# Kernel tuning notes

Hardware: AMD Instinct MI355X
Metric: run time of the kernel (lower is better)

Reference implementation:

```python
import jax, jax.numpy as jnp
import numpy as np

N, E = 50000, 640000
DIN, DH, DOUT = 128, 256, 128


def _glorot(k, i, o):
    return jax.random.normal(k, (i, o), jnp.float32) / np.sqrt(i)


def setup_inputs() -> dict:
    key = jax.random.key(0)
    ks = jax.random.split(key, 12)
    return {
        "x": jax.random.normal(ks[0], (N, DIN), jnp.float32),
        "edge_index": jax.random.randint(ks[1], (2, E), 0, N, dtype=jnp.int32),
        # SAGEConv 1: in -> hidden (lin_l on aggregated w/ bias, lin_r on root)
        "W1l": _glorot(ks[2], DIN, DH), "b1l": jnp.zeros((DH,), jnp.float32), "W1r": _glorot(ks[3], DIN, DH),
        "g1": jnp.ones((DH,), jnp.float32), "be1": jnp.zeros((DH,), jnp.float32),
        # skip projection (in != hidden)
        "Wsk": _glorot(ks[4], DIN, DH), "bsk": jnp.zeros((DH,), jnp.float32),
        # SAGEConv 2: hidden -> hidden
        "W2l": _glorot(ks[5], DH, DH), "b2l": jnp.zeros((DH,), jnp.float32), "W2r": _glorot(ks[6], DH, DH),
        "g2": jnp.ones((DH,), jnp.float32), "be2": jnp.zeros((DH,), jnp.float32),
        # SAGEConv 3: hidden -> out
        "W3l": _glorot(ks[7], DH, DOUT), "b3l": jnp.zeros((DOUT,), jnp.float32), "W3r": _glorot(ks[8], DH, DOUT),
    }


def _sage_conv(x, src, dst, Wl, bl, Wr, n):
    # mean aggregation of source features into destination nodes
    msg = x[src]                                                 # [E, d]
    agg = jax.ops.segment_sum(msg, dst, num_segments=n)          # [N, d]
    cnt = jax.ops.segment_sum(jnp.ones((src.shape[0],), x.dtype), dst, num_segments=n)
    agg = agg / jnp.maximum(cnt, 1.0)[:, None]
    return agg @ Wl + bl + x @ Wr


def _layernorm(x, g, b):
    mu = jnp.mean(x, axis=-1, keepdims=True)
    var = jnp.mean((x - mu) ** 2, axis=-1, keepdims=True)
    return (x - mu) * jax.lax.rsqrt(var + 1e-5) * g + b


def reference(x, edge_index, W1l, b1l, W1r, g1, be1, Wsk, bsk,
              W2l, b2l, W2r, g2, be2, W3l, b3l, W3r):
    src, dst = edge_index[0], edge_index[1]
    n = x.shape[0]
    # layer 0: conv -> LN -> relu -> (dropout p=0, eval) -> skip via projection
    h = _sage_conv(x, src, dst, W1l, b1l, W1r, n)
    h = jax.nn.relu(_layernorm(h, g1, be1))
    h = h + (x @ Wsk + bsk)
    # layer 1: conv -> LN -> relu -> residual add (shapes match)
    h2 = _sage_conv(h, src, dst, W2l, b2l, W2r, n)
    h2 = jax.nn.relu(_layernorm(h2, g2, be2)) + h
    # final conv (no norm/act)
    return _sage_conv(h2, src, dst, W3l, b3l, W3r, n)
```

## Files before the change

### kernel.cpp

```cpp
#include <hip/hip_runtime.h>


typedef float floatx4 __attribute__((ext_vector_type(4)));
typedef float floatx2 __attribute__((ext_vector_type(2)));
typedef short bf16x8 __attribute__((ext_vector_type(8)));

__device__ inline unsigned short f2bf(float f) {
    unsigned u = __float_as_uint(f);
    unsigned r = (u + 0x7fffu + ((u >> 16) & 1u)) >> 16;
    return (unsigned short)r;
}
__device__ inline float bf2f_lo(unsigned v) { return __uint_as_float(v << 16); }
__device__ inline float bf2f_hi(unsigned v) { return __uint_as_float(v & 0xffff0000u); }

__device__ inline void gl_lds16(const void* g, void* l) {
    __builtin_amdgcn_global_load_lds((const __attribute__((address_space(1))) unsigned int*)g,
                                     (__attribute__((address_space(3))) unsigned int*)l,
                                     16, 0, 0);
}

__global__ void hist_kernel(const int* __restrict__ dst, int* __restrict__ cnt, int E) {
    int i = blockIdx.x * blockDim.x + threadIdx.x;
    if (i < E) atomicAdd(&cnt[dst[i]], 1);
}

#define SCAN_CHUNK 2048

__global__ __launch_bounds__(256) void scan_blocksums(const int* __restrict__ cnt,
                                                      int* __restrict__ bsum, int N) {
    __shared__ int sh[256];
    int t = threadIdx.x;
    int base = blockIdx.x * SCAN_CHUNK + t * 8;
    int s = 0;
#pragma unroll
    for (int i = 0; i < 8; i++) {
        int idx = base + i;
        if (idx < N) s += cnt[idx];
    }
    sh[t] = s;
    __syncthreads();
    for (int off = 1; off < 256; off <<= 1) {
        int v = (t >= off) ? sh[t - off] : 0;
        __syncthreads();
        sh[t] += v;
        __syncthreads();
    }
    if (t == 255) bsum[blockIdx.x] = sh[255];
}

__global__ __launch_bounds__(256) void scan_bsums(const int* __restrict__ bsum,
                                                  int* __restrict__ boff, int NB,
                                                  int* __restrict__ rowptr, int N, int E) {
    __shared__ int sh[256];
    int t = threadIdx.x;
    int v = (t < NB) ? bsum[t] : 0;
    sh[t] = v;
    __syncthreads();
    for (int off = 1; off < 256; off <<= 1) {
        int u = (t >= off) ? sh[t - off] : 0;
        __syncthreads();
        sh[t] += u;
        __syncthreads();
    }
    if (t < NB) boff[t] = sh[t] - v;
    if (t == 0) rowptr[N] = E;
}

__global__ __launch_bounds__(256) void scan_final(const int* __restrict__ cnt,
                                                  const int* __restrict__ boff,
                                                  int* __restrict__ rowptr,
                                                  int* __restrict__ cursor,
                                                  float* __restrict__ invdeg, int N) {
    __shared__ int sh[256];
    int t = threadIdx.x;
    int base = blockIdx.x * SCAN_CHUNK + t * 8;
    int c[8];
    int s = 0;
#pragma unroll
    for (int i = 0; i < 8; i++) {
        int idx = base + i;
        c[i] = (idx < N) ? cnt[idx] : 0;
        s += c[i];
    }
    sh[t] = s;
    __syncthreads();
    for (int off = 1; off < 256; off <<= 1) {
        int v = (t >= off) ? sh[t - off] : 0;
        __syncthreads();
        sh[t] += v;
        __syncthreads();
    }
    int run = boff[blockIdx.x] + sh[t] - s;
#pragma unroll
    for (int i = 0; i < 8; i++) {
        int idx = base + i;
        if (idx < N) {
            rowptr[idx] = run;
            cursor[idx] = run;
            invdeg[idx] = 1.0f / (float)(c[i] > 1 ? c[i] : 1);
            run += c[i];
        }
    }
}

__global__ void scatter_kernel(const int* __restrict__ src, const int* __restrict__ dst,
                               int* __restrict__ cursor, int* __restrict__ col, int E) {
    int i = blockIdx.x * blockDim.x + threadIdx.x;
    if (i < E) {
        int p = atomicAdd(&cursor[dst[i]], 1);
        col[p] = src[i];
    }
}

__global__ void prep_weights(const float* __restrict__ W1l, const float* __restrict__ W1r,
                             const float* __restrict__ Wsk, const float* __restrict__ W2l,
                             const float* __restrict__ W2r, const float* __restrict__ W3l,
                             const float* __restrict__ W3r, const float* __restrict__ b1l,
                             const float* __restrict__ bsk,
                             unsigned short* __restrict__ WtC, unsigned short* __restrict__ Wt2,
                             unsigned short* __restrict__ Wt3, float* __restrict__ biasC) {
    int i = blockIdx.x * blockDim.x + threadIdx.x;
    if (i < 32768) {
        int k = i >> 8, n = i & 255;
        WtC[n * 256 + k] = f2bf(W1l[i]);
    } else if (i < 65536) {
        int j = i - 32768, k = j >> 8, n = j & 255;
        WtC[n * 256 + 128 + k] = f2bf(W1r[j]);
    } else if (i < 98304) {
        int j = i - 65536, k = j >> 8, n = j & 255;
        WtC[(256 + n) * 256 + 128 + k] = f2bf(Wsk[j]);
    } else if (i < 131072) {
        int j = i - 98304, k = j >> 8, n = j & 255;
        WtC[(256 + n) * 256 + k] = 0;
    } else if (i < 196608) {
        int j = i - 131072, k = j >> 8, n = j & 255;
        Wt2[n * 512 + k] = f2bf(W2l[j]);
    } else if (i < 262144) {
        int j = i - 196608, k = j >> 8, n = j & 255;
        Wt2[n * 512 + 256 + k] = f2bf(W2r[j]);
    } else if (i < 294912) {
        int j = i - 262144, k = j >> 7, n = j & 127;
        Wt3[n * 256 + k] = f2bf(W3l[j]);
    } else if (i < 327680) {
        int j = i - 294912, k = j >> 7, n = j & 127;
        Wt3[(128 + n) * 256 + k] = f2bf(W3r[j]);
    } else if (i < 328192) {
        int j = i - 327680;
        biasC[j] = (j < 256) ? b1l[j] : bsk[j - 256];
    }
}

__global__ void cvt_x2(const float* __restrict__ x, unsigned short* __restrict__ A1cat,
                       unsigned char* __restrict__ X8, int total32) {
    int i = blockIdx.x * blockDim.x + threadIdx.x;
    if (i >= total32) return;
    int r = i >> 5, c4 = (i & 31) * 4;
    float4 v = *(const float4*)(x + (size_t)r * 128 + c4);
    ushort4 o;
    o.x = f2bf(v.x); o.y = f2bf(v.y); o.z = f2bf(v.z); o.w = f2bf(v.w);
    *(ushort4*)(A1cat + (size_t)r * 256 + 128 + c4) = o;
    unsigned wpk = 0;
    wpk = __builtin_amdgcn_cvt_pk_fp8_f32(v.x, v.y, wpk, false);
    wpk = __builtin_amdgcn_cvt_pk_fp8_f32(v.z, v.w, wpk, true);
    *(unsigned*)(X8 + (size_t)r * 128 + c4) = wpk;
}

__device__ inline void accum_fp8(uint2 v, float m, float* a) {
    floatx2 p;
    p = __builtin_amdgcn_cvt_pk_f32_fp8(v.x, false); a[0] = fmaf(m, p.x, a[0]); a[1] = fmaf(m, p.y, a[1]);
    p = __builtin_amdgcn_cvt_pk_f32_fp8(v.x, true);  a[2] = fmaf(m, p.x, a[2]); a[3] = fmaf(m, p.y, a[3]);
    p = __builtin_amdgcn_cvt_pk_f32_fp8(v.y, false); a[4] = fmaf(m, p.x, a[4]); a[5] = fmaf(m, p.y, a[5]);
    p = __builtin_amdgcn_cvt_pk_f32_fp8(v.y, true);  a[6] = fmaf(m, p.x, a[6]); a[7] = fmaf(m, p.y, a[7]);
}

__global__ __launch_bounds__(256) void agg_fp8_128(const int* __restrict__ rowptr,
                                                   const int* __restrict__ col,
                                                   const float* __restrict__ invdeg,
                                                   const unsigned char* __restrict__ X8,
                                                   unsigned short* __restrict__ out, int ostride, int N) {
    int wid = (blockIdx.x * blockDim.x + threadIdx.x) >> 6;
    int lane = threadIdx.x & 63;
    if (wid >= N) return;
    int q = lane >> 4;
    int sub = lane & 15;
    const unsigned char* Xo = X8 + sub * 8;
    int s = rowptr[wid], e = rowptr[wid + 1];
    float a[8] = {0.f, 0.f, 0.f, 0.f, 0.f, 0.f, 0.f, 0.f};
    for (int j = s + q; j < e; j += 16) {
        int j1 = (j + 4 < e) ? j + 4 : j;
        int j2 = (j + 8 < e) ? j + 8 : j;
        int j3 = (j + 12 < e) ? j + 12 : j;
        float m1 = (j + 4 < e) ? 1.f : 0.f;
        float m2 = (j + 8 < e) ? 1.f : 0.f;
        float m3 = (j + 12 < e) ? 1.f : 0.f;
        int c0 = col[j], c1 = col[j1], c2 = col[j2], c3 = col[j3];
        uint2 v0 = *(const uint2*)(Xo + (size_t)c0 * 128);
        uint2 v1 = *(const uint2*)(Xo + (size_t)c1 * 128);
        uint2 v2 = *(const uint2*)(Xo + (size_t)c2 * 128);
        uint2 v3 = *(const uint2*)(Xo + (size_t)c3 * 128);
        accum_fp8(v0, 1.f, a);
        accum_fp8(v1, m1, a);
        accum_fp8(v2, m2, a);
        accum_fp8(v3, m3, a);
    }
#pragma unroll
    for (int i = 0; i < 8; i++) {
        a[i] += __shfl_xor(a[i], 16, 64);
        a[i] += __shfl_xor(a[i], 32, 64);
    }
    if (q == 0) {
        float inv = invdeg[wid];
        uint4 o;
        o.x = (unsigned)f2bf(a[0] * inv) | ((unsigned)f2bf(a[1] * inv) << 16);
        o.y = (unsigned)f2bf(a[2] * inv) | ((unsigned)f2bf(a[3] * inv) << 16);
        o.z = (unsigned)f2bf(a[4] * inv) | ((unsigned)f2bf(a[5] * inv) << 16);
        o.w = (unsigned)f2bf(a[6] * inv) | ((unsigned)f2bf(a[7] * inv) << 16);
        *(uint4*)(out + (size_t)wid * ostride + sub * 8) = o;
    }
}

__global__ __launch_bounds__(256) void agg_fp8_256(const int* __restrict__ rowptr,
                                                   const int* __restrict__ col,
                                                   const float* __restrict__ invdeg,
                                                   const unsigned char* __restrict__ H8,
                                                   unsigned short* __restrict__ out, int ostride, int N) {
    int wid = (blockIdx.x * blockDim.x + threadIdx.x) >> 6;
    int lane = threadIdx.x & 63;
    if (wid >= N) return;
    int half = lane >> 5;
    int sub = lane & 31;
    const unsigned char* Ho = H8 + sub * 8;
    int s = rowptr[wid], e = rowptr[wid + 1];
    float a[8] = {0.f, 0.f, 0.f, 0.f, 0.f, 0.f, 0.f, 0.f};
    for (int j = s + half; j < e; j += 8) {
        int j1 = (j + 2 < e) ? j + 2 : j;
        int j2 = (j + 4 < e) ? j + 4 : j;
        int j3 = (j + 6 < e) ? j + 6 : j;
        float m1 = (j + 2 < e) ? 1.f : 0.f;
        float m2 = (j + 4 < e) ? 1.f : 0.f;
        float m3 = (j + 6 < e) ? 1.f : 0.f;
        int c0 = col[j], c1 = col[j1], c2 = col[j2], c3 = col[j3];
        uint2 v0 = *(const uint2*)(Ho + (size_t)c0 * 256);
        uint2 v1 = *(const uint2*)(Ho + (size_t)c1 * 256);
        uint2 v2 = *(const uint2*)(Ho + (size_t)c2 * 256);
        uint2 v3 = *(const uint2*)(Ho + (size_t)c3 * 256);
        accum_fp8(v0, 1.f, a);
        accum_fp8(v1, m1, a);
        accum_fp8(v2, m2, a);
        accum_fp8(v3, m3, a);
    }
#pragma unroll
    for (int i = 0; i < 8; i++) a[i] += __shfl_xor(a[i], 32, 64);
    if (half == 0) {
        float inv = invdeg[wid];
        uint4 o;
        o.x = (unsigned)f2bf(a[0] * inv) | ((unsigned)f2bf(a[1] * inv) << 16);
        o.y = (unsigned)f2bf(a[2] * inv) | ((unsigned)f2bf(a[3] * inv) << 16);
        o.z = (unsigned)f2bf(a[4] * inv) | ((unsigned)f2bf(a[5] * inv) << 16);
        o.w = (unsigned)f2bf(a[6] * inv) | ((unsigned)f2bf(a[7] * inv) << 16);
        *(uint4*)(out + (size_t)wid * ostride + sub * 8) = o;
    }
}

__global__ __launch_bounds__(256) void agg_final_v3(const int* __restrict__ rowptr,
                                                    const int* __restrict__ col,
                                                    const float* __restrict__ invdeg,
                                                    const unsigned short* __restrict__ T,
                                                    const float* __restrict__ R,
                                                    float* __restrict__ out, int N) {
    int wid = (blockIdx.x * blockDim.x + threadIdx.x) >> 6;
    int lane = threadIdx.x & 63;
    if (wid >= N) return;
    int half = lane >> 5;
    int sub = lane & 31;
    const unsigned short* To = T + sub * 4;
    int s = rowptr[wid], e = rowptr[wid + 1];
    float a0 = 0.f, a1 = 0.f, a2 = 0.f, a3 = 0.f;
    for (int j = s + half; j < e; j += 8) {
        int j1 = (j + 2 < e) ? j + 2 : j;
        int j2 = (j + 4 < e) ? j + 4 : j;
        int j3 = (j + 6 < e) ? j + 6 : j;
        float m1 = (j + 2 < e) ? 1.f : 0.f;
        float m2 = (j + 4 < e) ? 1.f : 0.f;
        float m3 = (j + 6 < e) ? 1.f : 0.f;
        int c0 = col[j], c1 = col[j1], c2 = col[j2], c3 = col[j3];
        uint2 v0 = *(const uint2*)(To + (size_t)c0 * 128);
        uint2 v1 = *(const uint2*)(To + (size_t)c1 * 128);
        uint2 v2 = *(const uint2*)(To + (size_t)c2 * 128);
        uint2 v3 = *(const uint2*)(To + (size_t)c3 * 128);
        a0 += bf2f_lo(v0.x); a1 += bf2f_hi(v0.x); a2 += bf2f_lo(v0.y); a3 += bf2f_hi(v0.y);
        a0 = fmaf(m1, bf2f_lo(v1.x), a0); a1 = fmaf(m1, bf2f_hi(v1.x), a1);
        a2 = fmaf(m1, bf2f_lo(v1.y), a2); a3 = fmaf(m1, bf2f_hi(v1.y), a3);
        a0 = fmaf(m2, bf2f_lo(v2.x), a0); a1 = fmaf(m2, bf2f_hi(v2.x), a1);
        a2 = fmaf(m2, bf2f_lo(v2.y), a2); a3 = fmaf(m2, bf2f_hi(v2.y), a3);
        a0 = fmaf(m3, bf2f_lo(v3.x), a0); a1 = fmaf(m3, bf2f_hi(v3.x), a1);
        a2 = fmaf(m3, bf2f_lo(v3.y), a2); a3 = fmaf(m3, bf2f_hi(v3.y), a3);
    }
    a0 += __shfl_xor(a0, 32, 64);
    a1 += __shfl_xor(a1, 32, 64);
    a2 += __shfl_xor(a2, 32, 64);
    a3 += __shfl_xor(a3, 32, 64);
    if (half == 0) {
        float inv = invdeg[wid];
        float4 r = *(const float4*)(R + (size_t)wid * 128 + sub * 4);
        float4 o;
        o.x = a0 * inv + r.x;
        o.y = a1 * inv + r.y;
        o.z = a2 * inv + r.z;
        o.w = a3 * inv + r.w;
        *(float4*)(out + (size_t)wid * 128 + sub * 4) = o;
    }
}

template <int KIT, int NP, int SPLIT>
__global__ __launch_bounds__(256) void gemm_lds2(const unsigned short* __restrict__ A, int lda,
                                                 const unsigned short* __restrict__ B, int ldb,
                                                 const float* __restrict__ bias,
                                                 unsigned short* __restrict__ C0, int ldc0,
                                                 float* __restrict__ C1, int M) {
    constexpr int STAGE = 128 * 64 * 2;
    constexpr int SMEM_SZ = (STAGE * (1 + NP) > 34816) ? STAGE * (1 + NP) : 34816;
    __shared__ __align__(16) char smem[SMEM_SZ];
    unsigned short* sA = (unsigned short*)smem;
    int t = threadIdx.x;
    int lane = t & 63, w = t >> 6;
    int bm = blockIdx.x * 128;
    int bn0 = blockIdx.y * 128 * NP;
    int wm = (w >> 1) * 64, wn = (w & 1) * 64;
    int m16 = lane & 15, kq = lane >> 4;

    floatx4 acc[NP][4][4];
#pragma unroll
    for (int p = 0; p < NP; p++)
#pragma unroll
        for (int i = 0; i < 4; i++)
#pragma unroll
            for (int j = 0; j < 4; j++) acc[p][i][j] = (floatx4){0.f, 0.f, 0.f, 0.f};

    const int c_row = t >> 3;
    const int kc = (t & 7) ^ (c_row & 7);
    const int srcOff = kc * 8;
    const int fsw = (m16 & 7);

    for (int kt = 0; kt < KIT; kt++) {
        int k0 = kt * 64;
#pragma unroll
        for (int i = 0; i < 4; i++) {
            int rowA = bm + i * 32 + c_row;
            if (rowA > M - 1) rowA = M - 1;
            gl_lds16(A + (size_t)rowA * lda + k0 + srcOff, (void*)&sA[(size_t)(i * 256 + t) * 8]);
#pragma unroll
            for (int p = 0; p < NP; p++)
                gl_lds16(B + (size_t)(bn0 + p * 128 + i * 32 + c_row) * ldb + k0 + srcOff,
                         (void*)&sA[(size_t)((p + 1) * 128 * 64) + (size_t)(i * 256 + t) * 8]);
        }
        __syncthreads();
#pragma unroll
        for (int ks = 0; ks < 2; ks++) {
            int kcl = (ks << 2) | kq;
            bf16x8 af[4];
#pragma unroll
            for (int mi = 0; mi < 4; mi++)
                af[mi] = *(const bf16x8*)&sA[(wm + mi * 16 + m16) * 64 + (kcl ^ fsw) * 8];
#pragma unroll
            for (int p = 0; p < NP; p++) {
                const unsigned short* sB = sA + (p + 1) * 128 * 64;
                bf16x8 bfr[4];
#pragma unroll
                for (int ni = 0; ni < 4; ni++)
                    bfr[ni] = *(const bf16x8*)&sB[(wn + ni * 16 + m16) * 64 + (kcl ^ fsw) * 8];
#pragma unroll
                for (int mi = 0; mi < 4; mi++)
#pragma unroll
                    for (int ni = 0; ni < 4; ni++)
                        acc[p][mi][ni] =
                            __builtin_amdgcn_mfma_f32_16x16x32_bf16(af[mi], bfr[ni], acc[p][mi][ni], 0, 0, 0);
            }
        }
        __syncthreads();
    }

    float* wb = (float*)smem + w * (64 * 34);
#pragma unroll
    for (int p = 0; p < NP; p++) {
        const bool isF32 = (SPLIT == 1 && p == 1);
        const float* bp = (SPLIT == 0) ? (bias + bn0 + p * 128) : ((p == 0) ? nullptr : bias);
#pragma unroll
        for (int h = 0; h < 2; h++) {
#pragma unroll
            for (int nj = 0; nj < 2; nj++) {
                int ni = h * 2 + nj;
#pragma unroll
                for (int mi = 0; mi < 4; mi++)
#pragma unroll
                    for (int r = 0; r < 4; r++)
                        wb[(mi * 16 + kq * 4 + r) * 34 + nj * 16 + m16] = acc[p][mi][ni][r];
            }
            asm volatile("s_waitcnt lgkmcnt(0)" ::: "memory");
            if (!isF32) {
                int rsub = lane >> 2, c8 = (lane & 3) * 8;
                int ldc = (SPLIT == 0) ? ldc0 : 128;
                int lcol = wn + h * 32 + c8;
                int colbase = ((SPLIT == 0) ? bn0 + p * 128 : 0) + lcol;
                float bv[8];
#pragma unroll
                for (int j = 0; j < 8; j++) bv[j] = bp ? bp[lcol + j] : 0.f;
#pragma unroll
                for (int it = 0; it < 4; it++) {
                    int rr = it * 16 + rsub;
                    int grow = bm + wm + rr;
                    float v0 = wb[rr * 34 + c8 + 0] + bv[0];
                    float v1 = wb[rr * 34 + c8 + 1] + bv[1];
                    float v2 = wb[rr * 34 + c8 + 2] + bv[2];
                    float v3 = wb[rr * 34 + c8 + 3] + bv[3];
                    float v4 = wb[rr * 34 + c8 + 4] + bv[4];
                    float v5 = wb[rr * 34 + c8 + 5] + bv[5];
                    float v6 = wb[rr * 34 + c8 + 6] + bv[6];
                    float v7 = wb[rr * 34 + c8 + 7] + bv[7];
                    uint4 o;
                    o.x = (unsigned)f2bf(v0) | ((unsigned)f2bf(v1) << 16);
                    o.y = (unsigned)f2bf(v2) | ((unsigned)f2bf(v3) << 16);
                    o.z = (unsigned)f2bf(v4) | ((unsigned)f2bf(v5) << 16);
                    o.w = (unsigned)f2bf(v6) | ((unsigned)f2bf(v7) << 16);
                    if (grow < M) *(uint4*)(C0 + (size_t)grow * ldc + colbase) = o;
                }
            } else {
                int rsub = lane >> 3, c4 = (lane & 7) * 4;
                int gcol = wn + h * 32 + c4;
                float bv[4];
#pragma unroll
                for (int j = 0; j < 4; j++) bv[j] = bp[gcol + j];
#pragma unroll
                for (int it = 0; it < 8; it++) {
                    int rr = it * 8 + rsub;
                    int grow = bm + wm + rr;
                    float4 o;
                    o.x = wb[rr * 34 + c4 + 0] + bv[0];
                    o.y = wb[rr * 34 + c4 + 1] + bv[1];
                    o.z = wb[rr * 34 + c4 + 2] + bv[2];
                    o.w = wb[rr * 34 + c4 + 3] + bv[3];
                    if (grow < M) *(float4*)(C1 + (size_t)grow * 128 + gcol) = o;
                }
            }
            asm volatile("s_waitcnt lgkmcnt(0)" ::: "memory");
        }
    }
}

__global__ __launch_bounds__(256) void ln_fuse2(const unsigned short* __restrict__ u, int ustride,
                                                const unsigned short* __restrict__ a, int astride,
                                                const float* __restrict__ g, const float* __restrict__ b,
                                                unsigned short* __restrict__ out, int ostride,
                                                unsigned char* __restrict__ h8, int N) {
    int row = (blockIdx.x * blockDim.x + threadIdx.x) >> 6;
    int lane = threadIdx.x & 63;
    if (row >= N) return;
    uint2 uv = *(const uint2*)(u + (size_t)row * ustride + lane * 4);
    float v0 = bf2f_lo(uv.x), v1 = bf2f_hi(uv.x), v2 = bf2f_lo(uv.y), v3 = bf2f_hi(uv.y);
    float s = (v0 + v1) + (v2 + v3);
    float sq = (v0 * v0 + v1 * v1) + (v2 * v2 + v3 * v3);
    for (int off = 1; off < 64; off <<= 1) {
        s += __shfl_xor(s, off, 64);
        sq += __shfl_xor(sq, off, 64);
    }
    float mu = s * (1.f / 256.f);
    float var = sq * (1.f / 256.f) - mu * mu;
    float rs = rsqrtf(var + 1e-5f);
    float4 gv = *(const float4*)(g + lane * 4);
    float4 bv = *(const float4*)(b + lane * 4);
    uint2 av = *(const uint2*)(a + (size_t)row * astride + lane * 4);
    float a0 = bf2f_lo(av.x), a1 = bf2f_hi(av.x), a2 = bf2f_lo(av.y), a3 = bf2f_hi(av.y);
    float o0 = fmaxf((v0 - mu) * rs * gv.x + bv.x, 0.f) + a0;
    float o1 = fmaxf((v1 - mu) * rs * gv.y + bv.y, 0.f) + a1;
    float o2 = fmaxf((v2 - mu) * rs * gv.z + bv.z, 0.f) + a2;
    float o3 = fmaxf((v3 - mu) * rs * gv.w + bv.w, 0.f) + a3;
    ushort4 o;
    o.x = f2bf(o0); o.y = f2bf(o1); o.z = f2bf(o2); o.w = f2bf(o3);
    *(ushort4*)(out + (size_t)row * ostride + lane * 4) = o;
    if (h8) {
        unsigned wpk = 0;
        wpk = __builtin_amdgcn_cvt_pk_fp8_f32(o0, o1, wpk, false);
        wpk = __builtin_amdgcn_cvt_pk_fp8_f32(o2, o3, wpk, true);
        *(unsigned*)(h8 + (size_t)row * 256 + lane * 4) = wpk;
    }
}

extern "C" void kernel_launch(void* const* d_in, const int* in_sizes, int n_in,
                              void* d_out, int out_size, void* d_ws, size_t ws_size,
                              hipStream_t stream) {
    const float* x   = (const float*)d_in[0];
    const int*   ei  = (const int*)d_in[1];
    const float* W1l = (const float*)d_in[2];
    const float* b1l = (const float*)d_in[3];
    const float* W1r = (const float*)d_in[4];
    const float* g1  = (const float*)d_in[5];
    const float* be1 = (const float*)d_in[6];
    const float* Wsk = (const float*)d_in[7];
    const float* bsk = (const float*)d_in[8];
    const float* W2l = (const float*)d_in[9];
    const float* b2l = (const float*)d_in[10];
    const float* W2r = (const float*)d_in[11];
    const float* g2  = (const float*)d_in[12];
    const float* be2 = (const float*)d_in[13];
    const float* W3l = (const float*)d_in[14];
    const float* b3l = (const float*)d_in[15];
    const float* W3r = (const float*)d_in[16];

    const int N = in_sizes[0] / 128;
    const int E = in_sizes[1] / 2;
    const int* src = ei;
    const int* dst = ei + E;

    char* p = (char*)d_ws;
    auto alloc = [&](size_t bytes) {
        void* r = (void*)p;
        p += (bytes + 255) & ~(size_t)255;
        return r;
    };
    int*   cnt    = (int*)alloc(sizeof(int) * N);
    int*   rowptr = (int*)alloc(sizeof(int) * (N + 1));
    int*   cursor = (int*)alloc(sizeof(int) * N);
    float* invdeg = (float*)alloc(sizeof(float) * N);
    int*   col    = (int*)alloc(sizeof(int) * E);
    int*   bsum   = (int*)alloc(sizeof(int) * 256);
    int*   boff   = (int*)alloc(sizeof(int) * 256);
    unsigned short* A1cat = (unsigned short*)alloc(sizeof(short) * (size_t)N * 256);
    unsigned short* A2cat = (unsigned short*)alloc(sizeof(short) * (size_t)N * 512);
    unsigned short* U1    = (unsigned short*)alloc(sizeof(short) * (size_t)N * 512);
    float* r3 = (float*)alloc(sizeof(float) * (size_t)N * 128);
    unsigned char* H8 = (unsigned char*)alloc((size_t)N * 256);
    unsigned char* X8 = (unsigned char*)alloc((size_t)N * 128);
    unsigned short* WtC = (unsigned short*)alloc(sizeof(short) * 512 * 256);
    unsigned short* Wt2 = (unsigned short*)alloc(sizeof(short) * 256 * 512);
    unsigned short* Wt3 = (unsigned short*)alloc(sizeof(short) * 256 * 256);
    float* biasC = (float*)alloc(sizeof(float) * 512);
    unsigned short* t3 = A1cat;
    unsigned short* u2 = U1;

    hipMemsetAsync(cnt, 0, sizeof(int) * N, stream);
    hist_kernel<<<(E + 255) / 256, 256, 0, stream>>>(dst, cnt, E);
    int NB = (N + SCAN_CHUNK - 1) / SCAN_CHUNK;
    scan_blocksums<<<NB, 256, 0, stream>>>(cnt, bsum, N);
    scan_bsums<<<1, 256, 0, stream>>>(bsum, boff, NB, rowptr, N, E);
    scan_final<<<NB, 256, 0, stream>>>(cnt, boff, rowptr, cursor, invdeg, N);
    scatter_kernel<<<(E + 255) / 256, 256, 0, stream>>>(src, dst, cursor, col, E);

    prep_weights<<<(328192 + 255) / 256, 256, 0, stream>>>(W1l, W1r, Wsk, W2l, W2r, W3l, W3r,
                                                           b1l, bsk, WtC, Wt2, Wt3, biasC);
    cvt_x2<<<((N * 32) + 255) / 256, 256, 0, stream>>>(x, A1cat, X8, N * 32);

    int aggBlocks = (N + 3) / 4;
    int mBlocks = (N + 127) / 128;

    agg_fp8_128<<<aggBlocks, 256, 0, stream>>>(rowptr, col, invdeg, X8, A1cat, 256, N);
    gemm_lds2<4, 2, 0><<<dim3(mBlocks, 2), 256, 0, stream>>>(A1cat, 256, WtC, 256, biasC, U1, 512, nullptr, N);
    ln_fuse2<<<aggBlocks, 256, 0, stream>>>(U1, 512, U1 + 256, 512, g1, be1, A2cat + 256, 512, H8, N);

    agg_fp8_256<<<aggBlocks, 256, 0, stream>>>(rowptr, col, invdeg, H8, A2cat, 512, N);
    gemm_lds2<8, 2, 0><<<dim3(mBlocks, 1), 256, 0, stream>>>(A2cat, 512, Wt2, 512, b2l, u2, 256, nullptr, N);
    ln_fuse2<<<aggBlocks, 256, 0, stream>>>(u2, 256, A2cat + 256, 512, g2, be2, A2cat, 512, nullptr, N);

    gemm_lds2<4, 2, 1><<<dim3(mBlocks, 1), 256, 0, stream>>>(A2cat, 512, Wt3, 256, b3l, t3, 128, r3, N);
    agg_final_v3<<<aggBlocks, 256, 0, stream>>>(rowptr, col, invdeg, t3, r3, (float*)d_out, N);
}
```

Measured before the change: 384.3 us.

## Fuse LayerNorm/ReLU/residual epilogue into GEMM with full-width 512-thread tiles

```diff
diff --git a/kernel.cpp b/kernel.cpp
--- a/kernel.cpp
+++ b/kernel.cpp
@@ -312,176 +312,176 @@
     }
 }
 
-template <int KIT, int NP, int SPLIT>
-__global__ __launch_bounds__(256) void gemm_lds2(const unsigned short* __restrict__ A, int lda,
-                                                 const unsigned short* __restrict__ B, int ldb,
-                                                 const float* __restrict__ bias,
-                                                 unsigned short* __restrict__ C0, int ldc0,
-                                                 float* __restrict__ C1, int M) {
-    constexpr int STAGE = 128 * 64 * 2;
-    constexpr int SMEM_SZ = (STAGE * (1 + NP) > 34816) ? STAGE * (1 + NP) : 34816;
-    __shared__ __align__(16) char smem[SMEM_SZ];
-    unsigned short* sA = (unsigned short*)smem;
+template <int KIT, int NPAN, int MODE>
+__global__ __launch_bounds__(512) void gemm_fused(
+    const unsigned short* __restrict__ A, int lda,
+    const unsigned short* __restrict__ B, int ldb,
+    const float* __restrict__ bias,
+    const float* __restrict__ gamma, const float* __restrict__ beta,
+    const unsigned short* __restrict__ resid,
+    unsigned short* __restrict__ outb,
+    unsigned char* __restrict__ h8,
+    float* __restrict__ outf, int M) {
+    constexpr int COLS = NPAN * 256;
+    constexpr int LNW = COLS + 8;
+    constexpr int STAGE_E = 128 * 64;
+    constexpr int STAGE_F = 2 * STAGE_E / 2;
+    constexpr int SMEM_F = (STAGE_F > 32 * LNW) ? STAGE_F : 32 * LNW;
+    __shared__ __align__(16) float smemf[SMEM_F];
+    unsigned short* sbase = (unsigned short*)smemf;
+
     int t = threadIdx.x;
     int lane = t & 63, w = t >> 6;
     int bm = blockIdx.x * 128;
-    int bn0 = blockIdx.y * 128 * NP;
-    int wm = (w >> 1) * 64, wn = (w & 1) * 64;
+    int wm = (w & 1) * 64, wn = (w >> 1) * 64;
     int m16 = lane & 15, kq = lane >> 4;
 
-    floatx4 acc[NP][4][4];
-#pragma unroll
-    for (int p = 0; p < NP; p++)
+    floatx4 acc[NPAN][4][4];
+#pragma unroll
+    for (int p = 0; p < NPAN; p++)
 #pragma unroll
         for (int i = 0; i < 4; i++)
 #pragma unroll
             for (int j = 0; j < 4; j++) acc[p][i][j] = (floatx4){0.f, 0.f, 0.f, 0.f};
 
-    const int c_row = t >> 3;
-    const int kc = (t & 7) ^ (c_row & 7);
-    const int srcOff = kc * 8;
-    const int fsw = (m16 & 7);
-
+    const int s_row0 = t >> 3;
+    const int s_j = t & 7;
+
+    auto stage = [&](int kt, int bsel) {
+        unsigned short* s = sbase + bsel * STAGE_E;
+        int k0 = kt * 64;
+#pragma unroll
+        for (int i = 0; i < 2; i++) {
+            int row = s_row0 + i * 64;
+            int kc = s_j ^ (row & 7);
+            int rowA = bm + row;
+            if (rowA > M - 1) rowA = M - 1;
+            gl_lds16(A + (size_t)rowA * lda + k0 + kc * 8, (void*)&s[(size_t)(i * 512 + t) * 8]);
+        }
+    };
+
+    stage(0, 0);
+    __syncthreads();
     for (int kt = 0; kt < KIT; kt++) {
-        int k0 = kt * 64;
-#pragma unroll
-        for (int i = 0; i < 4; i++) {
-            int rowA = bm + i * 32 + c_row;
-            if (rowA > M - 1) rowA = M - 1;
-            gl_lds16(A + (size_t)rowA * lda + k0 + srcOff, (void*)&sA[(size_t)(i * 256 + t) * 8]);
-#pragma unroll
-            for (int p = 0; p < NP; p++)
-                gl_lds16(B + (size_t)(bn0 + p * 128 + i * 32 + c_row) * ldb + k0 + srcOff,
-                         (void*)&sA[(size_t)((p + 1) * 128 * 64) + (size_t)(i * 256 + t) * 8]);
-        }
-        __syncthreads();
+        if (kt + 1 < KIT) stage(kt + 1, (kt & 1) ^ 1);
+        const unsigned short* sA = sbase + (kt & 1) * STAGE_E;
 #pragma unroll
         for (int ks = 0; ks < 2; ks++) {
             int kcl = (ks << 2) | kq;
             bf16x8 af[4];
 #pragma unroll
             for (int mi = 0; mi < 4; mi++)
-                af[mi] = *(const bf16x8*)&sA[(wm + mi * 16 + m16) * 64 + (kcl ^ fsw) * 8];
-#pragma unroll
-            for (int p = 0; p < NP; p++) {
-                const unsigned short* sB = sA + (p + 1) * 128 * 64;
-                bf16x8 bfr[4];
+                af[mi] = *(const bf16x8*)&sA[(wm + mi * 16 + m16) * 64 + (kcl ^ (m16 & 7)) * 8];
+#pragma unroll
+            for (int p = 0; p < NPAN; p++) {
+                if (MODE == 0 && p == 1 && kt * 64 < 128) continue;
+                const unsigned short* Bp = B + (size_t)(wn + p * 256) * ldb + kt * 64;
+                bf16x8 bf[4];
 #pragma unroll
                 for (int ni = 0; ni < 4; ni++)
-                    bfr[ni] = *(const bf16x8*)&sB[(wn + ni * 16 + m16) * 64 + (kcl ^ fsw) * 8];
+                    bf[ni] = *(const bf16x8*)&Bp[(size_t)(ni * 16 + m16) * ldb + kcl * 8];
 #pragma unroll
                 for (int mi = 0; mi < 4; mi++)
 #pragma unroll
                     for (int ni = 0; ni < 4; ni++)
                         acc[p][mi][ni] =
-                            __builtin_amdgcn_mfma_f32_16x16x32_bf16(af[mi], bfr[ni], acc[p][mi][ni], 0, 0, 0);
+                            __builtin_amdgcn_mfma_f32_16x16x32_bf16(af[mi], bf[ni], acc[p][mi][ni], 0, 0, 0);
             }
         }
         __syncthreads();
     }
 
-    float* wb = (float*)smem + w * (64 * 34);
-#pragma unroll
-    for (int p = 0; p < NP; p++) {
-        const bool isF32 = (SPLIT == 1 && p == 1);
-        const float* bp = (SPLIT == 0) ? (bias + bn0 + p * 128) : ((p == 0) ? nullptr : bias);
-#pragma unroll
-        for (int h = 0; h < 2; h++) {
-#pragma unroll
-            for (int nj = 0; nj < 2; nj++) {
-                int ni = h * 2 + nj;
-#pragma unroll
-                for (int mi = 0; mi < 4; mi++)
-#pragma unroll
-                    for (int r = 0; r < 4; r++)
-                        wb[(mi * 16 + kq * 4 + r) * 34 + nj * 16 + m16] = acc[p][mi][ni][r];
-            }
-            asm volatile("s_waitcnt lgkmcnt(0)" ::: "memory");
-            if (!isF32) {
-                int rsub = lane >> 2, c8 = (lane & 3) * 8;
-                int ldc = (SPLIT == 0) ? ldc0 : 128;
-                int lcol = wn + h * 32 + c8;
-                int colbase = ((SPLIT == 0) ? bn0 + p * 128 : 0) + lcol;
-                float bv[8];
-#pragma unroll
-                for (int j = 0; j < 8; j++) bv[j] = bp ? bp[lcol + j] : 0.f;
-#pragma unroll
-                for (int it = 0; it < 4; it++) {
-                    int rr = it * 16 + rsub;
-                    int grow = bm + wm + rr;
-                    float v0 = wb[rr * 34 + c8 + 0] + bv[0];
-                    float v1 = wb[rr * 34 + c8 + 1] + bv[1];
-                    float v2 = wb[rr * 34 + c8 + 2] + bv[2];
-                    float v3 = wb[rr * 34 + c8 + 3] + bv[3];
-                    float v4 = wb[rr * 34 + c8 + 4] + bv[4];
-                    float v5 = wb[rr * 34 + c8 + 5] + bv[5];
-                    float v6 = wb[rr * 34 + c8 + 6] + bv[6];
-                    float v7 = wb[rr * 34 + c8 + 7] + bv[7];
-                    uint4 o;
-                    o.x = (unsigned)f2bf(v0) | ((unsigned)f2bf(v1) << 16);
-                    o.y = (unsigned)f2bf(v2) | ((unsigned)f2bf(v3) << 16);
-                    o.z = (unsigned)f2bf(v4) | ((unsigned)f2bf(v5) << 16);
-                    o.w = (unsigned)f2bf(v6) | ((unsigned)f2bf(v7) << 16);
-                    if (grow < M) *(uint4*)(C0 + (size_t)grow * ldc + colbase) = o;
+    float* lnb = smemf;
+    int c4 = lane * 4;
+    float4 bu = {0.f, 0.f, 0.f, 0.f}, bs = {0.f, 0.f, 0.f, 0.f};
+    float4 gv = {0.f, 0.f, 0.f, 0.f}, bv = {0.f, 0.f, 0.f, 0.f};
+    float4 b3 = {0.f, 0.f, 0.f, 0.f};
+    if (MODE == 0) {
+        bu = *(const float4*)&bias[c4];
+        bs = *(const float4*)&bias[256 + c4];
+        gv = *(const float4*)&gamma[c4];
+        bv = *(const float4*)&beta[c4];
+    } else if (MODE == 1) {
+        bu = *(const float4*)&bias[c4];
+        gv = *(const float4*)&gamma[c4];
+        bv = *(const float4*)&beta[c4];
+    } else {
+        if (lane >= 32) b3 = *(const float4*)&bias[c4 - 128];
+    }
+
+#pragma unroll
+    for (int g4 = 0; g4 < 4; g4++) {
+        if (wm == (g4 >> 1) * 64) {
+            int mi0 = (g4 & 1) * 2;
+#pragma unroll
+            for (int p = 0; p < NPAN; p++)
+#pragma unroll
+                for (int mm = 0; mm < 2; mm++)
+#pragma unroll
+                    for (int ni = 0; ni < 4; ni++)
+#pragma unroll
+                        for (int r = 0; r < 4; r++)
+                            lnb[(mm * 16 + kq * 4 + r) * LNW + wn + p * 256 + ni * 16 + m16] =
+                                acc[p][mi0 + mm][ni][r];
+        }
+        __syncthreads();
+#pragma unroll
+        for (int rr = 0; rr < 4; rr++) {
+            int lrow = w * 4 + rr;
+            int grow = bm + g4 * 32 + lrow;
+            bool valid = grow < M;
+            float4 u = *(const float4*)&lnb[lrow * LNW + c4];
+            if (MODE <= 1) {
+                u.x += bu.x; u.y += bu.y; u.z += bu.z; u.w += bu.w;
+                float s1 = (u.x + u.y) + (u.z + u.w);
+                float s2 = (u.x * u.x + u.y * u.y) + (u.z * u.z + u.w * u.w);
+#pragma unroll
+                for (int off = 1; off < 64; off <<= 1) {
+                    s1 += __shfl_xor(s1, off, 64);
+                    s2 += __shfl_xor(s2, off, 64);
+                }
+                float mu = s1 * (1.f / 256.f);
+                float var = s2 * (1.f / 256.f) - mu * mu;
+                float rs = rsqrtf(var + 1e-5f);
+                float a0, a1, a2, a3;
+                if (MODE == 0) {
+                    float4 sv = *(const float4*)&lnb[lrow * LNW + 256 + c4];
+                    a0 = sv.x + bs.x; a1 = sv.y + bs.y; a2 = sv.z + bs.z; a3 = sv.w + bs.w;
+                } else {
+                    int gr = valid ? grow : M - 1;
+                    uint2 hv = *(const uint2*)(resid + (size_t)gr * 512 + c4);
+                    a0 = bf2f_lo(hv.x); a1 = bf2f_hi(hv.x); a2 = bf2f_lo(hv.y); a3 = bf2f_hi(hv.y);
+                }
+                float o0 = fmaxf((u.x - mu) * rs * gv.x + bv.x, 0.f) + a0;
+                float o1 = fmaxf((u.y - mu) * rs * gv.y + bv.y, 0.f) + a1;
+                float o2 = fmaxf((u.z - mu) * rs * gv.z + bv.z, 0.f) + a2;
+                float o3 = fmaxf((u.w - mu) * rs * gv.w + bv.w, 0.f) + a3;
+                if (valid) {
+                    ushort4 o;
+                    o.x = f2bf(o0); o.y = f2bf(o1); o.z = f2bf(o2); o.w = f2bf(o3);
+                    *(ushort4*)(outb + (size_t)grow * 512 + c4) = o;
+                    if (MODE == 0) {
+                        unsigned wpk = 0;
+                        wpk = __builtin_amdgcn_cvt_pk_fp8_f32(o0, o1, wpk, false);
+                        wpk = __builtin_amdgcn_cvt_pk_fp8_f32(o2, o3, wpk, true);
+                        *(unsigned*)(h8 + (size_t)grow * 256 + c4) = wpk;
+                    }
                 }
             } else {
-                int rsub = lane >> 3, c4 = (lane & 7) * 4;
-                int gcol = wn + h * 32 + c4;
-                float bv[4];
-#pragma unroll
-                for (int j = 0; j < 4; j++) bv[j] = bp[gcol + j];
-#pragma unroll
-                for (int it = 0; it < 8; it++) {
-                    int rr = it * 8 + rsub;
-                    int grow = bm + wm + rr;
-                    float4 o;
-                    o.x = wb[rr * 34 + c4 + 0] + bv[0];
-                    o.y = wb[rr * 34 + c4 + 1] + bv[1];
-                    o.z = wb[rr * 34 + c4 + 2] + bv[2];
-                    o.w = wb[rr * 34 + c4 + 3] + bv[3];
-                    if (grow < M) *(float4*)(C1 + (size_t)grow * 128 + gcol) = o;
+                if (valid) {
+                    if (lane < 32) {
+                        ushort4 o;
+                        o.x = f2bf(u.x); o.y = f2bf(u.y); o.z = f2bf(u.z); o.w = f2bf(u.w);
+                        *(ushort4*)(outb + (size_t)grow * 128 + c4) = o;
+                    } else {
+                        float4 o;
+                        o.x = u.x + b3.x; o.y = u.y + b3.y; o.z = u.z + b3.z; o.w = u.w + b3.w;
+                        *(float4*)(outf + (size_t)grow * 128 + (c4 - 128)) = o;
+                    }
                 }
             }
-            asm volatile("s_waitcnt lgkmcnt(0)" ::: "memory");
         }
-    }
-}
-
-__global__ __launch_bounds__(256) void ln_fuse2(const unsigned short* __restrict__ u, int ustride,
-                                                const unsigned short* __restrict__ a, int astride,
-                                                const float* __restrict__ g, const float* __restrict__ b,
-                                                unsigned short* __restrict__ out, int ostride,
-                                                unsigned char* __restrict__ h8, int N) {
-    int row = (blockIdx.x * blockDim.x + threadIdx.x) >> 6;
-    int lane = threadIdx.x & 63;
-    if (row >= N) return;
-    uint2 uv = *(const uint2*)(u + (size_t)row * ustride + lane * 4);
-    float v0 = bf2f_lo(uv.x), v1 = bf2f_hi(uv.x), v2 = bf2f_lo(uv.y), v3 = bf2f_hi(uv.y);
-    float s = (v0 + v1) + (v2 + v3);
-    float sq = (v0 * v0 + v1 * v1) + (v2 * v2 + v3 * v3);
-    for (int off = 1; off < 64; off <<= 1) {
-        s += __shfl_xor(s, off, 64);
-        sq += __shfl_xor(sq, off, 64);
-    }
-    float mu = s * (1.f / 256.f);
-    float var = sq * (1.f / 256.f) - mu * mu;
-    float rs = rsqrtf(var + 1e-5f);
-    float4 gv = *(const float4*)(g + lane * 4);
-    float4 bv = *(const float4*)(b + lane * 4);
-    uint2 av = *(const uint2*)(a + (size_t)row * astride + lane * 4);
-    float a0 = bf2f_lo(av.x), a1 = bf2f_hi(av.x), a2 = bf2f_lo(av.y), a3 = bf2f_hi(av.y);
-    float o0 = fmaxf((v0 - mu) * rs * gv.x + bv.x, 0.f) + a0;
-    float o1 = fmaxf((v1 - mu) * rs * gv.y + bv.y, 0.f) + a1;
-    float o2 = fmaxf((v2 - mu) * rs * gv.z + bv.z, 0.f) + a2;
-    float o3 = fmaxf((v3 - mu) * rs * gv.w + bv.w, 0.f) + a3;
-    ushort4 o;
-    o.x = f2bf(o0); o.y = f2bf(o1); o.z = f2bf(o2); o.w = f2bf(o3);
-    *(ushort4*)(out + (size_t)row * ostride + lane * 4) = o;
-    if (h8) {
-        unsigned wpk = 0;
-        wpk = __builtin_amdgcn_cvt_pk_fp8_f32(o0, o1, wpk, false);
-        wpk = __builtin_amdgcn_cvt_pk_fp8_f32(o2, o3, wpk, true);
-        *(unsigned*)(h8 + (size_t)row * 256 + lane * 4) = wpk;
+        __syncthreads();
     }
 }
 
@@ -526,7 +526,6 @@
     int*   boff   = (int*)alloc(sizeof(int) * 256);
     unsigned short* A1cat = (unsigned short*)alloc(sizeof(short) * (size_t)N * 256);
     unsigned short* A2cat = (unsigned short*)alloc(sizeof(short) * (size_t)N * 512);
-    unsigned short* U1    = (unsigned short*)alloc(sizeof(short) * (size_t)N * 512);
     float* r3 = (float*)alloc(sizeof(float) * (size_t)N * 128);
     unsigned char* H8 = (unsigned char*)alloc((size_t)N * 256);
     unsigned char* X8 = (unsigned char*)alloc((size_t)N * 128);
@@ -535,7 +534,6 @@
     unsigned short* Wt3 = (unsigned short*)alloc(sizeof(short) * 256 * 256);
     float* biasC = (float*)alloc(sizeof(float) * 512);
     unsigned short* t3 = A1cat;
-    unsigned short* u2 = U1;
 
     hipMemsetAsync(cnt, 0, sizeof(int) * N, stream);
     hist_kernel<<<(E + 255) / 256, 256, 0, stream>>>(dst, cnt, E);
@@ -553,13 +551,14 @@
     int mBlocks = (N + 127) / 128;
 
     agg_fp8_128<<<aggBlocks, 256, 0, stream>>>(rowptr, col, invdeg, X8, A1cat, 256, N);
-    gemm_lds2<4, 2, 0><<<dim3(mBlocks, 2), 256, 0, stream>>>(A1cat, 256, WtC, 256, biasC, U1, 512, nullptr, N);
-    ln_fuse2<<<aggBlocks, 256, 0, stream>>>(U1, 512, U1 + 256, 512, g1, be1, A2cat + 256, 512, H8, N);
+    gemm_fused<4, 2, 0><<<mBlocks, 512, 0, stream>>>(A1cat, 256, WtC, 256, biasC, g1, be1,
+                                                     nullptr, A2cat + 256, H8, nullptr, N);
 
     agg_fp8_256<<<aggBlocks, 256, 0, stream>>>(rowptr, col, invdeg, H8, A2cat, 512, N);
-    gemm_lds2<8, 2, 0><<<dim3(mBlocks, 1), 256, 0, stream>>>(A2cat, 512, Wt2, 512, b2l, u2, 256, nullptr, N);
-    ln_fuse2<<<aggBlocks, 256, 0, stream>>>(u2, 256, A2cat + 256, 512, g2, be2, A2cat, 512, nullptr, N);
-
-    gemm_lds2<4, 2, 1><<<dim3(mBlocks, 1), 256, 0, stream>>>(A2cat, 512, Wt3, 256, b3l, t3, 128, r3, N);
+    gemm_fused<8, 1, 1><<<mBlocks, 512, 0, stream>>>(A2cat, 512, Wt2, 512, b2l, g2, be2,
+                                                     A2cat + 256, A2cat, nullptr, nullptr, N);
+
+    gemm_fused<4, 1, 2><<<mBlocks, 512, 0, stream>>>(A2cat, 512, Wt3, 256, b3l, nullptr, nullptr,
+                                                     nullptr, t3, nullptr, r3, N);
     agg_final_v3<<<aggBlocks, 256, 0, stream>>>(rowptr, col, invdeg, t3, r3, (float*)d_out, N);
 }
```

Measured after the change: 388.3 us. About the same (+1.0%).
